# Performance work log

Measured on AMD Instinct MI355X. Metric: run time of the kernel, lower is better.

Reference implementation:

```python
import jax, jax.numpy as jnp
import numpy as np

B, N1, N2, D, H = 16, 1024, 1024, 1024, 16
DH = D // H  # head dim = 64
NEG = jnp.float32(-1e30)  # mask fill value (avoids -inf NaNs, bf16-safe)


def setup_inputs() -> dict:
    key = jax.random.key(0)
    ks = jax.random.split(key, 8)
    s = 0.02
    q = jax.random.normal(ks[0], (B, N1, D), dtype=jnp.float32)
    x = jax.random.normal(ks[1], (B, N2, D), dtype=jnp.float32)
    Wq = jax.random.normal(ks[2], (D, D), dtype=jnp.float32) * s
    Wk = jax.random.normal(ks[3], (D, D), dtype=jnp.float32) * s
    Wv = jax.random.normal(ks[4], (D, D), dtype=jnp.float32) * s
    Wo = jax.random.normal(ks[5], (D, D), dtype=jnp.float32) * s
    bq = jnp.zeros((D,), jnp.float32)
    bk = jnp.zeros((D,), jnp.float32)
    bv = jnp.zeros((D,), jnp.float32)
    bo = jnp.zeros((D,), jnp.float32)
    adj_mat = jax.random.randint(ks[6], (N1, N2), 0, 2).astype(jnp.bool_)
    return {"q": q, "x": x, "Wq": Wq, "bq": bq, "Wk": Wk, "bk": bk,
            "Wv": Wv, "bv": bv, "Wo": Wo, "bo": bo, "adj_mat": adj_mat}


def reference(q, x, Wq, bq, Wk, bk, Wv, bv, Wo, bo, adj_mat):
    b = q.shape[0]
    # QKV projections (torch Linear: y = x @ W.T + b), split into heads
    qh = (q @ Wq.T + bq).reshape(b, N1, H, DH).transpose(0, 2, 1, 3)  # [B,H,N1,DH]
    kh = (x @ Wk.T + bk).reshape(b, N2, H, DH).transpose(0, 2, 1, 3)  # [B,H,N2,DH]
    vh = (x @ Wv.T + bv).reshape(b, N2, H, DH).transpose(0, 2, 1, 3)  # [B,H,N2,DH]
    # masked SDPA with fixed adjacency mask (broadcast over batch & heads)
    scale = jnp.asarray(DH, qh.dtype) ** -0.5
    scores = jnp.einsum("bhqd,bhkd->bhqk", qh, kh) * scale           # [B,H,N1,N2]
    scores = jnp.where(adj_mat, scores, NEG)
    attn = jax.nn.softmax(scores, axis=-1)
    o = jnp.einsum("bhqk,bhkd->bhqd", attn, vh)                      # [B,H,N1,DH]
    o = o.transpose(0, 2, 1, 3).reshape(b, N1, D)
    return o @ Wo.T + bo
```

## Files before the change

kernel.cpp:

```cpp
#include <hip/hip_runtime.h>


typedef float f32x4 __attribute__((ext_vector_type(4)));
typedef float f32x16 __attribute__((ext_vector_type(16)));
typedef __bf16 bf16x8 __attribute__((ext_vector_type(8)));

#define QSCALE 0.18033688f

__device__ __forceinline__ unsigned short f2bf(float f) {
    unsigned u = __builtin_bit_cast(unsigned, f);
    unsigned r = u + 0x7fffu + ((u >> 16) & 1u);
    return (unsigned short)(r >> 16);
}
__device__ __forceinline__ unsigned pk2(float a, float b) {
    return (unsigned)f2bf(a) | ((unsigned)f2bf(b) << 16);
}

__global__ __launch_bounds__(256) void cvt_bf16(const float* __restrict__ src,
                                                unsigned short* __restrict__ dst,
                                                int n8) {
    const int idx = blockIdx.x * 256 + threadIdx.x;
    if (idx >= n8) return;
    float4 a = ((const float4*)src)[idx * 2];
    float4 b = ((const float4*)src)[idx * 2 + 1];
    uint4 u;
    u.x = pk2(a.x, a.y); u.y = pk2(a.z, a.w);
    u.z = pk2(b.x, b.y); u.w = pk2(b.z, b.w);
    ((uint4*)dst)[idx] = u;
}

__global__ __launch_bounds__(256) void cvt_w4(const float* __restrict__ W0,
                                              const float* __restrict__ W1,
                                              const float* __restrict__ W2,
                                              const float* __restrict__ W3,
                                              unsigned short* __restrict__ o0,
                                              unsigned short* __restrict__ o1,
                                              unsigned short* __restrict__ o2,
                                              unsigned short* __restrict__ o3) {
    const float* s = (blockIdx.y == 0) ? W0 : (blockIdx.y == 1) ? W1
                   : (blockIdx.y == 2) ? W2 : W3;
    unsigned short* d = (blockIdx.y == 0) ? o0 : (blockIdx.y == 1) ? o1
                      : (blockIdx.y == 2) ? o2 : o3;
    const int idx = blockIdx.x * 256 + threadIdx.x;
    float4 a = ((const float4*)s)[idx * 2];
    float4 b = ((const float4*)s)[idx * 2 + 1];
    uint4 u;
    u.x = pk2(a.x, a.y); u.y = pk2(a.z, a.w);
    u.z = pk2(b.x, b.y); u.w = pk2(b.z, b.w);
    ((uint4*)d)[idx] = u;
}

template <int OUTM>
__global__ __launch_bounds__(256) void gemm_lds(const unsigned short* __restrict__ A,
                                                const unsigned short* __restrict__ W,
                                                const float* __restrict__ bias,
                                                void* __restrict__ Cp,
                                                float scale) {
    constexpr int N = 1024, K = 1024;
    __shared__ unsigned short As[128 * 64];
    __shared__ unsigned short Bs[128 * 64];

    const int t    = threadIdx.x;
    const int wave = t >> 6;
    const int lane = t & 63;
    const int bid  = blockIdx.x;
    const int xcd  = bid & 7;
    const int jj   = bid >> 3;
    const int n0   = (jj & 7) * 128;
    const int m0   = (xcd * 16 + (jj >> 3)) * 128;
    const int wr   = (wave >> 1) * 64;
    const int wc   = (wave & 1) * 64;
    const int lm   = lane & 15;
    const int quad = lane >> 4;

    int aoff[4], boff[4];
#pragma unroll
    for (int i = 0; i < 4; i++) {
        const int slot = wave * 256 + i * 64 + lane;
        const int r = slot >> 3;
        const int csrc = (slot & 7) ^ (r & 7);
        aoff[i] = (m0 + r) * K + csrc * 8;
        boff[i] = (n0 + r) * K + csrc * 8;
    }

    f32x4 acc[4][4] = {};

    for (int k0 = 0; k0 < K; k0 += 64) {
#pragma unroll
        for (int i = 0; i < 4; i++) {
            __builtin_amdgcn_global_load_lds(
                (const __attribute__((address_space(1))) unsigned int*)(A + aoff[i] + k0),
                (__attribute__((address_space(3))) unsigned int*)((char*)As + wave * 4096 + i * 1024),
                16, 0, 0);
            __builtin_amdgcn_global_load_lds(
                (const __attribute__((address_space(1))) unsigned int*)(W + boff[i] + k0),
                (__attribute__((address_space(3))) unsigned int*)((char*)Bs + wave * 4096 + i * 1024),
                16, 0, 0);
        }
        __syncthreads();

        bf16x8 af[2][4], bfr[2][4];
#pragma unroll
        for (int ks = 0; ks < 2; ks++)
#pragma unroll
            for (int i = 0; i < 4; i++) {
                const int pos = ((ks * 4 + quad) ^ (lm & 7)) * 16;
                af[ks][i]  = *(const bf16x8*)((const char*)As + (wr + i * 16 + lm) * 128 + pos);
                bfr[ks][i] = *(const bf16x8*)((const char*)Bs + (wc + i * 16 + lm) * 128 + pos);
            }
#pragma unroll
        for (int ks = 0; ks < 2; ks++)
#pragma unroll
            for (int i = 0; i < 4; i++)
#pragma unroll
                for (int j = 0; j < 4; j++)
                    acc[i][j] = __builtin_amdgcn_mfma_f32_16x16x32_bf16(af[ks][i], bfr[ks][j],
                                                                        acc[i][j], 0, 0, 0);
        __syncthreads();
    }

#pragma unroll
    for (int i = 0; i < 4; i++) {
        const int row = m0 + wr + i * 16 + quad * 4;
#pragma unroll
        for (int j = 0; j < 4; j++) {
            const int col = n0 + wc + j * 16 + lm;
            const float bb = bias[col];
            if constexpr (OUTM == 2) {
                const int bi = row >> 10, n2 = row & 1023;
                const int hh = col >> 6, dh = col & 63;
                uint2 pkd;
                pkd.x = pk2((acc[i][j][0] + bb) * scale, (acc[i][j][1] + bb) * scale);
                pkd.y = pk2((acc[i][j][2] + bb) * scale, (acc[i][j][3] + bb) * scale);
                *(uint2*)&((unsigned short*)Cp)[((size_t)((bi * 16 + hh) * 64 + dh) << 10) + n2] = pkd;
            } else {
#pragma unroll
                for (int rr = 0; rr < 4; rr++) {
                    const float v = (acc[i][j][rr] + bb) * scale;
                    if constexpr (OUTM == 0)
                        ((unsigned short*)Cp)[(size_t)(row + rr) * N + col] = f2bf(v);
                    else
                        ((float*)Cp)[(size_t)(row + rr) * N + col] = v;
                }
            }
        }
    }
}

template <bool A_BF16, int OUTM>
__global__ __launch_bounds__(256) void gemm_bt(const void* __restrict__ Ap,
                                               const float* __restrict__ Wp,
                                               const float* __restrict__ bias,
                                               void* __restrict__ Cp,
                                               float scale) {
    constexpr int N = 1024, K = 1024;
    __shared__ unsigned short As[128 * 40];
    __shared__ unsigned short Bs[128 * 40];

    const int t    = threadIdx.x;
    const int n0   = blockIdx.x * 128;
    const int m0   = blockIdx.y * 128;
    const int wave = t >> 6;
    const int lane = t & 63;
    const int wr   = (wave >> 1) * 64;
    const int wc   = (wave & 1) * 64;
    const int lm   = lane & 15;
    const int quad = lane >> 4;
    const int kfr  = quad * 8;
    const int srow  = t >> 1;
    const int shalf = (t & 1) * 16;

    f32x4 acc[4][4] = {};

    for (int k0 = 0; k0 < K; k0 += 32) {
        {
            unsigned short* dst = &As[srow * 40 + shalf];
            if constexpr (A_BF16) {
                const unsigned short* pa =
                    (const unsigned short*)Ap + (size_t)(m0 + srow) * K + k0 + shalf;
                *(uint4*)dst       = *(const uint4*)pa;
                *(uint4*)(dst + 8) = *(const uint4*)(pa + 8);
            } else {
                const float* pa = (const float*)Ap + (size_t)(m0 + srow) * K + k0 + shalf;
                float4 f0 = *(const float4*)(pa + 0);
                float4 f1 = *(const float4*)(pa + 4);
                float4 f2 = *(const float4*)(pa + 8);
                float4 f3 = *(const float4*)(pa + 12);
                uint4 u0, u1;
                u0.x = pk2(f0.x, f0.y); u0.y = pk2(f0.z, f0.w);
                u0.z = pk2(f1.x, f1.y); u0.w = pk2(f1.z, f1.w);
                u1.x = pk2(f2.x, f2.y); u1.y = pk2(f2.z, f2.w);
                u1.z = pk2(f3.x, f3.y); u1.w = pk2(f3.z, f3.w);
                *(uint4*)dst       = u0;
                *(uint4*)(dst + 8) = u1;
            }
        }
        {
            const float* pb = Wp + (size_t)(n0 + srow) * K + k0 + shalf;
            float4 f0 = *(const float4*)(pb + 0);
            float4 f1 = *(const float4*)(pb + 4);
            float4 f2 = *(const float4*)(pb + 8);
            float4 f3 = *(const float4*)(pb + 12);
            uint4 u0, u1;
            u0.x = pk2(f0.x, f0.y); u0.y = pk2(f0.z, f0.w);
            u0.z = pk2(f1.x, f1.y); u0.w = pk2(f1.z, f1.w);
            u1.x = pk2(f2.x, f2.y); u1.y = pk2(f2.z, f2.w);
            u1.z = pk2(f3.x, f3.y); u1.w = pk2(f3.z, f3.w);
            unsigned short* dst = &Bs[srow * 40 + shalf];
            *(uint4*)dst       = u0;
            *(uint4*)(dst + 8) = u1;
        }
        __syncthreads();

        bf16x8 af[4], bfr[4];
#pragma unroll
        for (int i = 0; i < 4; i++)
            af[i] = *reinterpret_cast<const bf16x8*>(&As[(wr + i * 16 + lm) * 40 + kfr]);
#pragma unroll
        for (int j = 0; j < 4; j++)
            bfr[j] = *reinterpret_cast<const bf16x8*>(&Bs[(wc + j * 16 + lm) * 40 + kfr]);
#pragma unroll
        for (int i = 0; i < 4; i++)
#pragma unroll
            for (int j = 0; j < 4; j++)
                acc[i][j] = __builtin_amdgcn_mfma_f32_16x16x32_bf16(af[i], bfr[j],
                                                                    acc[i][j], 0, 0, 0);
        __syncthreads();
    }

#pragma unroll
    for (int i = 0; i < 4; i++) {
        const int row = m0 + wr + i * 16 + quad * 4;
#pragma unroll
        for (int j = 0; j < 4; j++) {
            const int col = n0 + wc + j * 16 + lm;
            const float bb = bias[col];
#pragma unroll
            for (int rr = 0; rr < 4; rr++) {
                const float v = (acc[i][j][rr] + bb) * scale;
                const int m = row + rr;
                if constexpr (OUTM == 0) {
                    ((unsigned short*)Cp)[(size_t)m * N + col] = f2bf(v);
                } else if constexpr (OUTM == 1) {
                    ((float*)Cp)[(size_t)m * N + col] = v;
                } else {
                    const int bi = m >> 10, n2 = m & 1023;
                    const int hh = col >> 6, dh = col & 63;
                    ((unsigned short*)Cp)[((size_t)((bi * 16 + hh) * 64 + dh) << 10) + n2] =
                        f2bf(v);
                }
            }
        }
    }
}

__global__ __launch_bounds__(256) void pack_adj(const int* __restrict__ adj,
                                                unsigned* __restrict__ adjm) {
    const int idx = blockIdx.x * 256 + threadIdx.x;
    const int* src = adj + (size_t)idx * 32;
    unsigned w = 0;
#pragma unroll
    for (int i = 0; i < 32; i++) w |= (src[i] != 0 ? 1u : 0u) << i;
    adjm[idx] = w;
}

__global__ __launch_bounds__(256, 3) void attn_kernel(const unsigned short* __restrict__ Q,
                                                      const unsigned short* __restrict__ K,
                                                      const unsigned short* __restrict__ Vt,
                                                      const unsigned* __restrict__ adjm,
                                                      unsigned short* __restrict__ O) {
    __shared__ unsigned short Kbuf[2][4096];
    __shared__ unsigned short Vbuf[2][4096];

    const int t    = threadIdx.x;
    const int wave = t >> 6;
    const int lane = t & 63;
    const int l32  = lane & 31;
    const int hi   = lane >> 5;

    const int bid   = blockIdx.x;
    const int xcd   = bid & 7;
    const int jj    = bid >> 3;
    const int group = xcd * 32 + (jj >> 3);
    const int q0    = (jj & 7) * 128;
    const int h     = group & 15;
    const int b     = group >> 4;

    const int qrow = q0 + wave * 32 + l32;

    int    ldofs[2];
    size_t kofs[2], vofs[2];
#pragma unroll
    for (int i = 0; i < 2; i++) {
        const int slot = i * 256 + t;
        const int r    = slot >> 3;
        const int cs   = (slot & 7) ^ (r & 7);
        ldofs[i] = slot * 16;
        kofs[i]  = (size_t)(b * 1024 + r) * 1024 + h * 64 + cs * 8;
        vofs[i]  = ((size_t)((b * 16 + h) * 64 + r) << 10) + cs * 8;
    }

    bf16x8 aq[4];
    {
        const unsigned short* qp =
            Q + ((size_t)(b * 1024 + qrow) * 1024 + h * 64 + hi * 8);
#pragma unroll
        for (int s = 0; s < 4; s++)
            aq[s] = __builtin_bit_cast(bf16x8, *(const uint4*)(qp + s * 16));
    }

    bf16x8 bones;
    {
        uint4 u; u.x = 0x3F803F80u; u.y = u.x; u.z = u.x; u.w = u.x;
        bones = __builtin_bit_cast(bf16x8, u);
    }

    f32x16 of0 = {}, of1 = {}, ol = {};

    auto STAGE = [&](int bi, int c) {
        const size_t j0 = (size_t)c * 64;
#pragma unroll
        for (int i = 0; i < 2; i++) {
            __builtin_amdgcn_global_load_lds(
                (const __attribute__((address_space(1))) unsigned int*)(K + kofs[i] + j0 * 1024),
                (__attribute__((address_space(3))) unsigned int*)((char*)&Kbuf[bi][0] + ldofs[i]),
                16, 0, 0);
            __builtin_amdgcn_global_load_lds(
                (const __attribute__((address_space(1))) unsigned int*)(Vt + vofs[i] + j0),
                (__attribute__((address_space(3))) unsigned int*)((char*)&Vbuf[bi][0] + ldofs[i]),
                16, 0, 0);
        }
    };

    STAGE(0, 0);
    __syncthreads();

    int bi = 0;
    for (int c = 0; c < 16; ++c) {
        const uint2 mw = *(const uint2*)&adjm[(size_t)qrow * 32 + c * 2];

        if (c < 15) STAGE(bi ^ 1, c + 1);

        f32x16 sf[2] = {{}, {}};
        __builtin_amdgcn_s_setprio(1);
#pragma unroll
        for (int f = 0; f < 2; f++)
#pragma unroll
            for (int s = 0; s < 4; s++) {
                const int pos = ((2 * s + hi) ^ (l32 & 7)) * 16;
                const bf16x8 kf =
                    *(const bf16x8*)((const char*)&Kbuf[bi][0] + (f * 32 + l32) * 128 + pos);
                sf[f] = __builtin_amdgcn_mfma_f32_32x32x16_bf16(kf, aq[s], sf[f], 0, 0, 0);
            }
        __builtin_amdgcn_s_setprio(0);

        unsigned d[2][4][2];
#pragma unroll
        for (int f = 0; f < 2; f++) {
            const unsigned wh = ((f == 0) ? mw.x : mw.y) >> (hi * 4);
            float p[16];
#pragma unroll
            for (int r = 0; r < 16; r++) {
                const unsigned bit = (wh >> ((r & 3) + 8 * (r >> 2))) & 1u;
                p[r] = __builtin_amdgcn_exp2f(bit ? sf[f][r] : -1e30f);
            }
#pragma unroll
            for (int a = 0; a < 4; a++)
#pragma unroll
                for (int bb = 0; bb < 2; bb++) {
                    unsigned dd;
                    asm("v_cvt_pk_bf16_f32 %0, %1, %2"
                        : "=v"(dd) : "v"(p[4 * a + 2 * bb]), "v"(p[4 * a + 2 * bb + 1]));
                    d[f][a][bb] = dd;
                }
        }

        bf16x8 tA[4];
#pragma unroll
        for (int s = 0; s < 4; s++) {
            const int f = s >> 1, sg = s & 1;
            unsigned A0 = d[f][2 * sg][0], B0 = d[f][2 * sg + 1][0];
            unsigned A1 = d[f][2 * sg][1], B1 = d[f][2 * sg + 1][1];
            asm("v_permlane32_swap_b32 %0, %1" : "+v"(A0), "+v"(B0));
            asm("v_permlane32_swap_b32 %0, %1" : "+v"(A1), "+v"(B1));
            uint4 td; td.x = A0; td.y = A1; td.z = B0; td.w = B1;
            tA[s] = __builtin_bit_cast(bf16x8, td);
        }

        __builtin_amdgcn_s_setprio(1);
#pragma unroll
        for (int s = 0; s < 4; s++) {
            const int pos = ((2 * s + hi) ^ (l32 & 7)) * 16;
            const bf16x8 v0 = *(const bf16x8*)((const char*)&Vbuf[bi][0] + l32 * 128 + pos);
            const bf16x8 v1 = *(const bf16x8*)((const char*)&Vbuf[bi][0] + (32 + l32) * 128 + pos);
            of0 = __builtin_amdgcn_mfma_f32_32x32x16_bf16(tA[s], v0, of0, 0, 0, 0);
            of1 = __builtin_amdgcn_mfma_f32_32x32x16_bf16(tA[s], v1, of1, 0, 0, 0);
            ol  = __builtin_amdgcn_mfma_f32_32x32x16_bf16(tA[s], bones, ol, 0, 0, 0);
        }
        __builtin_amdgcn_s_setprio(0);

        __syncthreads();
        bi ^= 1;
    }

#pragma unroll
    for (int r = 0; r < 16; r++) {
        const float iv = 1.0f / ol[r];
        const size_t row = (size_t)(b * 1024 + q0 + wave * 32 +
                                    (r & 3) + 8 * (r >> 2) + 4 * hi);
        unsigned short* op = O + row * 1024 + h * 64 + l32;
        op[0]  = f2bf(of0[r] * iv);
        op[32] = f2bf(of1[r] * iv);
    }
}

extern "C" void kernel_launch(void* const* d_in, const int* in_sizes, int n_in,
                              void* d_out, int out_size, void* d_ws, size_t ws_size,
                              hipStream_t stream) {
    const float* q  = (const float*)d_in[0];
    const float* x  = (const float*)d_in[1];
    const float* Wq = (const float*)d_in[2];
    const float* bq = (const float*)d_in[3];
    const float* Wk = (const float*)d_in[4];
    const float* bk = (const float*)d_in[5];
    const float* Wv = (const float*)d_in[6];
    const float* bv = (const float*)d_in[7];
    const float* Wo = (const float*)d_in[8];
    const float* bo = (const float*)d_in[9];
    const int* adj  = (const int*)d_in[10];
    float* out = (float*)d_out;

    const size_t MB = 1024 * 1024;
    const size_t NELEM = (size_t)16 * MB;
    char* w = (char*)d_ws;

    dim3 gswz(1024), tb(256);
    const size_t FULL_WS = 168 * MB + 128 * 1024;

    if (ws_size >= FULL_WS) {
        unsigned short* qb  = (unsigned short*)(w);
        unsigned short* xb  = (unsigned short*)(w + 32 * MB);
        unsigned short* Wqb = (unsigned short*)(w + 64 * MB);
        unsigned short* Wkb = (unsigned short*)(w + 66 * MB);
        unsigned short* Wvb = (unsigned short*)(w + 68 * MB);
        unsigned short* Wob = (unsigned short*)(w + 70 * MB);
        unsigned short* Qb  = (unsigned short*)(w + 72 * MB);
        unsigned short* Kb  = (unsigned short*)(w + 104 * MB);
        unsigned short* Vtb = (unsigned short*)(w + 136 * MB);
        unsigned* adjm      = (unsigned*)(w + 168 * MB);
        unsigned short* Ob  = qb;

        hipLaunchKernelGGL(cvt_bf16, dim3(8192), tb, 0, stream, q, qb, (int)(NELEM / 8));
        hipLaunchKernelGGL(cvt_bf16, dim3(8192), tb, 0, stream, x, xb, (int)(NELEM / 8));
        hipLaunchKernelGGL(cvt_w4, dim3(512, 4), tb, 0, stream, Wq, Wk, Wv, Wo,
                           Wqb, Wkb, Wvb, Wob);
        hipLaunchKernelGGL(pack_adj, dim3(128), tb, 0, stream, adj, adjm);

        hipLaunchKernelGGL((gemm_lds<0>), gswz, tb, 0, stream, qb, Wqb, bq, (void*)Qb, QSCALE);
        hipLaunchKernelGGL((gemm_lds<0>), gswz, tb, 0, stream, xb, Wkb, bk, (void*)Kb, 1.0f);
        hipLaunchKernelGGL((gemm_lds<2>), gswz, tb, 0, stream, xb, Wvb, bv, (void*)Vtb, 1.0f);
        hipLaunchKernelGGL(attn_kernel, dim3(2048), tb, 0, stream, Qb, Kb, Vtb, adjm, Ob);
        hipLaunchKernelGGL((gemm_lds<1>), gswz, tb, 0, stream, Ob, Wob, bo, (void*)out, 1.0f);
    } else {
        unsigned short* Qb  = (unsigned short*)(w);
        unsigned short* Kb  = (unsigned short*)(w + 32 * MB);
        unsigned short* Vtb = (unsigned short*)(w + 64 * MB);
        unsigned short* Ob  = (unsigned short*)(w + 96 * MB);
        unsigned* adjm      = (unsigned*)(w + 128 * MB);

        hipLaunchKernelGGL(pack_adj, dim3(128), tb, 0, stream, adj, adjm);
        hipLaunchKernelGGL((gemm_bt<false, 0>), dim3(8, 128), tb, 0, stream,
                           (const void*)q, Wq, bq, (void*)Qb, QSCALE);
        hipLaunchKernelGGL((gemm_bt<false, 0>), dim3(8, 128), tb, 0, stream,
                           (const void*)x, Wk, bk, (void*)Kb, 1.0f);
        hipLaunchKernelGGL((gemm_bt<false, 2>), dim3(8, 128), tb, 0, stream,
                           (const void*)x, Wv, bv, (void*)Vtb, 1.0f);
        hipLaunchKernelGGL(attn_kernel, dim3(2048), tb, 0, stream, Qb, Kb, Vtb, adjm, Ob);
        hipLaunchKernelGGL((gemm_bt<true, 1>), dim3(8, 128), tb, 0, stream,
                           (const void*)Ob, Wo, bo, (void*)out, 1.0f);
    }
}
```

Baseline: 474.9 us.

## Double-buffer GEMM LDS tiles, merge input conversions, pad attention LDS buffers

The projection GEMM now keeps two LDS stages and issues the global-to-LDS loads for the next K tile before computing on the current one. The goal is to hide global load latency behind MFMA work. The change doubles LDS use per block, and launch bounds now ask for two blocks per CU. It also folds the two activation bf16 conversions into one launch and pads the attention K/V LDS buffers, which presumably targets bank conflicts.

```diff
diff --git a/kernel.cpp b/kernel.cpp
--- a/kernel.cpp
+++ b/kernel.cpp
@@ -16,11 +16,13 @@
     return (unsigned)f2bf(a) | ((unsigned)f2bf(b) << 16);
 }
 
-__global__ __launch_bounds__(256) void cvt_bf16(const float* __restrict__ src,
-                                                unsigned short* __restrict__ dst,
-                                                int n8) {
+__global__ __launch_bounds__(256) void cvt_bf16(const float* __restrict__ s0,
+                                                unsigned short* __restrict__ d0,
+                                                const float* __restrict__ s1,
+                                                unsigned short* __restrict__ d1) {
+    const float* src = blockIdx.y ? s1 : s0;
+    unsigned short* dst = blockIdx.y ? d1 : d0;
     const int idx = blockIdx.x * 256 + threadIdx.x;
-    if (idx >= n8) return;
     float4 a = ((const float4*)src)[idx * 2];
     float4 b = ((const float4*)src)[idx * 2 + 1];
     uint4 u;
@@ -51,14 +53,14 @@
 }
 
 template <int OUTM>
-__global__ __launch_bounds__(256) void gemm_lds(const unsigned short* __restrict__ A,
+__global__ __launch_bounds__(256, 2) void gemm2(const unsigned short* __restrict__ A,
                                                 const unsigned short* __restrict__ W,
                                                 const float* __restrict__ bias,
                                                 void* __restrict__ Cp,
                                                 float scale) {
     constexpr int N = 1024, K = 1024;
-    __shared__ unsigned short As[128 * 64];
-    __shared__ unsigned short Bs[128 * 64];
+    __shared__ unsigned short As[2][128 * 64];
+    __shared__ unsigned short Bs[2][128 * 64];
 
     const int t    = threadIdx.x;
     const int wave = t >> 6;
@@ -83,21 +85,28 @@
         boff[i] = (n0 + r) * K + csrc * 8;
     }
 
-    f32x4 acc[4][4] = {};
-
-    for (int k0 = 0; k0 < K; k0 += 64) {
+    auto STAGE = [&](int cb, int k0) {
 #pragma unroll
         for (int i = 0; i < 4; i++) {
             __builtin_amdgcn_global_load_lds(
                 (const __attribute__((address_space(1))) unsigned int*)(A + aoff[i] + k0),
-                (__attribute__((address_space(3))) unsigned int*)((char*)As + wave * 4096 + i * 1024),
+                (__attribute__((address_space(3))) unsigned int*)((char*)&As[cb][0] + wave * 4096 + i * 1024),
                 16, 0, 0);
             __builtin_amdgcn_global_load_lds(
                 (const __attribute__((address_space(1))) unsigned int*)(W + boff[i] + k0),
-                (__attribute__((address_space(3))) unsigned int*)((char*)Bs + wave * 4096 + i * 1024),
+                (__attribute__((address_space(3))) unsigned int*)((char*)&Bs[cb][0] + wave * 4096 + i * 1024),
                 16, 0, 0);
         }
-        __syncthreads();
+    };
+
+    f32x4 acc[4][4] = {};
+
+    STAGE(0, 0);
+    __syncthreads();
+
+    int cur = 0;
+    for (int k0 = 0; k0 < K; k0 += 64) {
+        if (k0 + 64 < K) STAGE(cur ^ 1, k0 + 64);
 
         bf16x8 af[2][4], bfr[2][4];
 #pragma unroll
@@ -105,8 +114,8 @@
 #pragma unroll
             for (int i = 0; i < 4; i++) {
                 const int pos = ((ks * 4 + quad) ^ (lm & 7)) * 16;
-                af[ks][i]  = *(const bf16x8*)((const char*)As + (wr + i * 16 + lm) * 128 + pos);
-                bfr[ks][i] = *(const bf16x8*)((const char*)Bs + (wc + i * 16 + lm) * 128 + pos);
+                af[ks][i]  = *(const bf16x8*)((const char*)&As[cur][0] + (wr + i * 16 + lm) * 128 + pos);
+                bfr[ks][i] = *(const bf16x8*)((const char*)&Bs[cur][0] + (wc + i * 16 + lm) * 128 + pos);
             }
 #pragma unroll
         for (int ks = 0; ks < 2; ks++)
@@ -117,6 +126,7 @@
                     acc[i][j] = __builtin_amdgcn_mfma_f32_16x16x32_bf16(af[ks][i], bfr[ks][j],
                                                                         acc[i][j], 0, 0, 0);
         __syncthreads();
+        cur ^= 1;
     }
 
 #pragma unroll
@@ -269,8 +279,8 @@
                                                       const unsigned short* __restrict__ Vt,
                                                       const unsigned* __restrict__ adjm,
                                                       unsigned short* __restrict__ O) {
-    __shared__ unsigned short Kbuf[2][4096];
-    __shared__ unsigned short Vbuf[2][4096];
+    __shared__ unsigned short Kbuf[2][4112];
+    __shared__ unsigned short Vbuf[2][4112];
 
     const int t    = threadIdx.x;
     const int wave = t >> 6;
@@ -431,7 +441,6 @@
     float* out = (float*)d_out;
 
     const size_t MB = 1024 * 1024;
-    const size_t NELEM = (size_t)16 * MB;
     char* w = (char*)d_ws;
 
     dim3 gswz(1024), tb(256);
@@ -450,17 +459,16 @@
         unsigned* adjm      = (unsigned*)(w + 168 * MB);
         unsigned short* Ob  = qb;
 
-        hipLaunchKernelGGL(cvt_bf16, dim3(8192), tb, 0, stream, q, qb, (int)(NELEM / 8));
-        hipLaunchKernelGGL(cvt_bf16, dim3(8192), tb, 0, stream, x, xb, (int)(NELEM / 8));
+        hipLaunchKernelGGL(cvt_bf16, dim3(8192, 2), tb, 0, stream, q, qb, x, xb);
         hipLaunchKernelGGL(cvt_w4, dim3(512, 4), tb, 0, stream, Wq, Wk, Wv, Wo,
                            Wqb, Wkb, Wvb, Wob);
         hipLaunchKernelGGL(pack_adj, dim3(128), tb, 0, stream, adj, adjm);
 
-        hipLaunchKernelGGL((gemm_lds<0>), gswz, tb, 0, stream, qb, Wqb, bq, (void*)Qb, QSCALE);
-        hipLaunchKernelGGL((gemm_lds<0>), gswz, tb, 0, stream, xb, Wkb, bk, (void*)Kb, 1.0f);
-        hipLaunchKernelGGL((gemm_lds<2>), gswz, tb, 0, stream, xb, Wvb, bv, (void*)Vtb, 1.0f);
+        hipLaunchKernelGGL((gemm2<0>), gswz, tb, 0, stream, qb, Wqb, bq, (void*)Qb, QSCALE);
+        hipLaunchKernelGGL((gemm2<0>), gswz, tb, 0, stream, xb, Wkb, bk, (void*)Kb, 1.0f);
+        hipLaunchKernelGGL((gemm2<2>), gswz, tb, 0, stream, xb, Wvb, bv, (void*)Vtb, 1.0f);
         hipLaunchKernelGGL(attn_kernel, dim3(2048), tb, 0, stream, Qb, Kb, Vtb, adjm, Ob);
-        hipLaunchKernelGGL((gemm_lds<1>), gswz, tb, 0, stream, Ob, Wob, bo, (void*)out, 1.0f);
+        hipLaunchKernelGGL((gemm2<1>), gswz, tb, 0, stream, Ob, Wob, bo, (void*)out, 1.0f);
     } else {
         unsigned short* Qb  = (unsigned short*)(w);
         unsigned short* Kb  = (unsigned short*)(w + 32 * MB);
```

New measurement: 448.9 us. -5.5%, faster.
